# Kernel optimization log

Measured on AMD Instinct MI355X. Metric: run time of the kernel, lower is better.

## Reference

```python
import jax, jax.numpy as jnp
import numpy as np

N, M, P, K = 2, 131072, 1024, 4
C_TP, H_TP, W_TP = 32, 256, 256
PDIM, ODIM = 32, 32


def _harmonic(x, n=4):
    # pytorch3d HarmonicEmbedding: freqs 2^i, cat([sin, cos, x])
    freqs = 2.0 ** jnp.arange(n, dtype=x.dtype)
    e = (x[..., None] * freqs).reshape(x.shape[:-1] + (x.shape[-1] * n,))
    return jnp.concatenate([jnp.sin(e), jnp.cos(e), x], axis=-1)


def _normalize(x, eps=1e-12):
    return x / jnp.maximum(jnp.linalg.norm(x, axis=-1, keepdims=True), eps)


def _lin(x, w, b):
    return x @ w + b


def _grid_sample(img, gx, gy):
    # img [B,C,H,W]; gx,gy [B,Hg,Wg] in [-1,1]; bilinear, zeros pad, align_corners=False
    B, C, H, W = img.shape
    ix = ((gx + 1.0) * W - 1.0) / 2.0
    iy = ((gy + 1.0) * H - 1.0) / 2.0
    x0 = jnp.floor(ix); y0 = jnp.floor(iy)
    x1 = x0 + 1.0; y1 = y0 + 1.0
    wa = (x1 - ix) * (y1 - iy); wb = (ix - x0) * (y1 - iy)
    wc = (x1 - ix) * (iy - y0); wd = (ix - x0) * (iy - y0)
    b = jnp.arange(B)[:, None, None]

    def gather(xi, yi):
        xi = xi.astype(jnp.int32); yi = yi.astype(jnp.int32)
        valid = (xi >= 0) & (xi < W) & (yi >= 0) & (yi < H)
        xc = jnp.clip(xi, 0, W - 1); yc = jnp.clip(yi, 0, H - 1)
        v = img[b, :, yc, xc]  # [B,Hg,Wg,C]
        return v * valid[..., None]

    return (gather(x0, y0) * wa[..., None] + gather(x1, y0) * wb[..., None]
            + gather(x0, y1) * wc[..., None] + gather(x1, y1) * wd[..., None])


def _sample_from_planes_mean(coords, tplanes):
    # coords [N,M,3]; tplanes [N,3,C,H,W]; plane projections (x,y),(x,z),(z,y)
    n, m, _ = coords.shape
    _, n_pl, c, h, w = tplanes.shape
    proj = jnp.stack([coords[..., jnp.array([0, 1])],
                      coords[..., jnp.array([0, 2])],
                      coords[..., jnp.array([2, 1])]], axis=1)  # [N,3,M,2]
    proj = proj.reshape(n * n_pl, 1, m, 2)
    planes = tplanes.reshape(n * n_pl, c, h, w)
    out = _grid_sample(planes, proj[..., 0], proj[..., 1])  # [N*3,1,M,C]
    return out.reshape(n, n_pl, m, c).mean(axis=1)  # [N,M,C]


def _forward(coordinates, directions, points_position, tex_tplanes, pts_emb,
             q_w1, q_b1, q_w2, q_b2, f_w1, f_b1, f_w2, f_b2, f_w3, f_b3,
             d_w, d_b, r_w1, r_b1, r_w2, r_b2):
    selector = jnp.all((coordinates > -1.0) & (coordinates < 1.0), axis=-1)  # [N,M]
    tex = _sample_from_planes_mean(coordinates, tex_tplanes)  # [N,M,32]

    # KNN (squared distances, sorted ascending) via ||a||^2+||b||^2-2ab
    a2 = jnp.sum(coordinates * coordinates, -1)  # [N,M]
    b2 = jnp.sum(points_position * points_position, -1)  # [N,P]
    d2 = a2[:, :, None] + b2[:, None, :] - 2.0 * jnp.einsum('nmc,npc->nmp', coordinates, points_position)
    neg, idx = jax.lax.top_k(-d2, K)
    dist = -neg  # [N,M,K]
    bidx = jnp.arange(coordinates.shape[0])[:, None, None]
    nn = points_position[bidx, idx]  # [N,M,K,3]
    pf = pts_emb[idx]  # [N,M,K,32]
    rel = _normalize(coordinates[:, :, None] - nn)
    pe = _harmonic(rel)  # [N,M,K,27]
    h = jnp.concatenate([pf, pe], axis=-1)
    h = jax.nn.relu(_lin(h, q_w1, q_b1))
    h = _lin(h, q_w2, q_b2)  # [N,M,K,32]
    wgt = 1.0 / dist
    wgt = wgt / jnp.sum(wgt, axis=1, keepdims=True)  # note: dim=1 as in original
    pts_feat = jnp.sum(h * wgt[..., None], axis=2)  # [N,M,32]

    feat = jnp.concatenate([tex, pts_feat], axis=-1)
    feat = jax.nn.relu(_lin(feat, f_w1, f_b1))
    feat = jax.nn.relu(_lin(feat, f_w2, f_b2))
    feat = _lin(feat, f_w3, f_b3)  # [N,M,128]

    raw = (jax.nn.softplus(10.0 * _lin(feat, d_w, d_b)) / 10.0) * selector[..., None]
    densities = 1.0 - jnp.exp(-raw)

    rays = _harmonic(_normalize(directions))  # [N,M,27]
    rgb = jax.nn.relu(_lin(jnp.concatenate([feat, rays], axis=-1), r_w1, r_b1))
    rgb = _lin(rgb, r_w2, r_b2)
    r3 = jax.nn.sigmoid(rgb[..., :3]) * (1.0 + 2 * 0.001) - 0.001
    rgb = jnp.concatenate([r3, rgb[..., 3:]], axis=-1)
    return densities, rgb, dist


def setup_inputs() -> dict:
    keys = iter(jax.random.split(jax.random.key(0), 40))

    def nrm(shape, s=1.0):
        return jax.random.normal(next(keys), shape, jnp.float32) * s

    def lin_p(fin, fout):
        s = 1.0 / np.sqrt(fin)
        return nrm((fin, fout), s), nrm((fout,), s)

    coordinates = jax.random.uniform(next(keys), (N, M, 3), jnp.float32, -1.0, 1.0)
    directions = nrm((N, M, 3))
    points_position = jax.random.uniform(next(keys), (N, P, 3), jnp.float32, -1.0, 1.0)
    tex_tplanes = nrm((N, 3, C_TP, H_TP, W_TP))
    pts_emb = nrm((P, PDIM), 0.02)
    q_w1, q_b1 = lin_p(PDIM + 27, ODIM * 2)
    q_w2, q_b2 = lin_p(ODIM * 2, ODIM)
    f_w1, f_b1 = lin_p(64, 128)
    f_w2, f_b2 = lin_p(128, 128)
    f_w3, f_b3 = lin_p(128, 128)
    d_w, d_b = lin_p(128, 1)
    r_w1, r_b1 = lin_p(128 + 27, 64)
    r_w2, r_b2 = lin_p(64, 3)
    return dict(coordinates=coordinates, directions=directions,
                points_position=points_position, tex_tplanes=tex_tplanes,
                pts_emb=pts_emb, q_w1=q_w1, q_b1=q_b1, q_w2=q_w2, q_b2=q_b2,
                f_w1=f_w1, f_b1=f_b1, f_w2=f_w2, f_b2=f_b2, f_w3=f_w3, f_b3=f_b3,
                d_w=d_w, d_b=d_b, r_w1=r_w1, r_b1=r_b1, r_w2=r_w2, r_b2=r_b2)


def reference(coordinates, directions, points_position, tex_tplanes, pts_emb,
              q_w1, q_b1, q_w2, q_b2, f_w1, f_b1, f_w2, f_b2, f_w3, f_b3,
              d_w, d_b, r_w1, r_b1, r_w2, r_b2):
    return _forward(coordinates, directions, points_position, tex_tplanes, pts_emb,
                    q_w1, q_b1, q_w2, q_b2, f_w1, f_b1, f_w2, f_b2, f_w3, f_b3,
                    d_w, d_b, r_w1, r_b1, r_w2, r_b2)
```

## Files before the change

kernel.cpp:

```cpp
#include <hip/hip_runtime.h>

constexpr int MQ   = 131072;
constexpr int NPTS = 1024;

constexpr size_t WS_PTS4 = 4096;

__device__ __forceinline__ float np_sq3(float x, float y, float z){
  #pragma clang fp contract(off)
  float s = (x*x + y*y) + z*z;
  return s;
}
__device__ __forceinline__ float np_d2(float a2, float b2,
                                       float c0, float c1, float c2,
                                       float p0, float p1, float p2){
  #pragma clang fp contract(off)
  float dot = (c0*p0 + c1*p1) + c2*p2;
  float d   = (a2 + b2) - 2.0f*dot;
  return d;
}

__global__ void k_err_r15(float code, float* __restrict__ out){
  out[0] = code;
}

__global__ __launch_bounds__(256) void k_prep_r15(const float* __restrict__ pts,
                                                  float4* __restrict__ pts4,
                                                  float* __restrict__ denom){
  int i = blockIdx.x*256 + threadIdx.x;
  if (i < 8) denom[i] = 0.f;
  if (i < 2*NPTS){
    float x = pts[i*3+0], y = pts[i*3+1], z = pts[i*3+2];
    pts4[i] = make_float4(x, y, z, np_sq3(x,y,z));
  }
}

__global__ __launch_bounds__(256) void k_denom_r15(const float* __restrict__ coords,
                                                   const float4* __restrict__ pts4,
                                                   float* __restrict__ denom){
  __shared__ float red[4][4];
  int n = blockIdx.y;
  int m = blockIdx.x*256 + threadIdx.x;
  size_t g = (size_t)n*MQ + m;
  float c0 = coords[g*3+0], c1 = coords[g*3+1], c2 = coords[g*3+2];
  float a2 = np_sq3(c0,c1,c2);
  const float4* pp = pts4 + n*NPTS;
  float bd0=1e30f,bd1=1e30f,bd2=1e30f,bd3=1e30f;
  for (int p = 0; p < NPTS; ++p){
    float4 q = pp[p];
    float d = np_d2(a2, q.w, c0,c1,c2, q.x,q.y,q.z);
    if (d < bd3){
      if (d < bd2){
        bd3=bd2;
        if (d < bd1){ bd2=bd1; if (d < bd0){ bd1=bd0; bd0=d; } else bd1=d; }
        else bd2=d;
      } else bd3=d;
    }
  }
  float w0 = 1.f/bd0, w1 = 1.f/bd1, w2 = 1.f/bd2, w3 = 1.f/bd3;
  #pragma unroll
  for (int off=32; off>0; off>>=1){
    w0 += __shfl_down(w0, off); w1 += __shfl_down(w1, off);
    w2 += __shfl_down(w2, off); w3 += __shfl_down(w3, off);
  }
  int lane = threadIdx.x & 63, wv = threadIdx.x >> 6;
  if (lane == 0){ red[wv][0]=w0; red[wv][1]=w1; red[wv][2]=w2; red[wv][3]=w3; }
  __syncthreads();
  if (threadIdx.x < 4){
    int k = threadIdx.x;
    atomicAdd(&denom[n*4+k], red[0][k]+red[1][k]+red[2][k]+red[3][k]);
  }
}

template<int IN, int OUT, bool RELU>
__device__ __forceinline__ void layer_s(const float* in, float* out,
                                        const float* __restrict__ gw,
                                        const float* __restrict__ gb){
  #pragma unroll
  for (int jb = 0; jb < OUT/8; ++jb){
    float a[8];
    #pragma unroll
    for (int j=0;j<8;++j) a[j] = gb[jb*8+j];
    #pragma unroll
    for (int i = 0; i < IN; ++i){
      float x = in[i];
      #pragma unroll
      for (int j=0;j<8;++j) a[j] = fmaf(x, gw[i*OUT + jb*8 + j], a[j]);
    }
    #pragma unroll
    for (int j=0;j<8;++j) out[jb*8+j] = RELU ? fmaxf(a[j],0.f) : a[j];
  }
}

__global__ __launch_bounds__(256, 2) void k_main_r15(
    const float* __restrict__ coords, const float* __restrict__ dirs,
    const float* __restrict__ planes, const float* __restrict__ pemb,
    const float* __restrict__ qw1, const float* __restrict__ qb1,
    const float* __restrict__ qw2, const float* __restrict__ qb2,
    const float* __restrict__ fw1, const float* __restrict__ fb1,
    const float* __restrict__ fw2, const float* __restrict__ fb2,
    const float* __restrict__ fw3, const float* __restrict__ fb3,
    const float* __restrict__ dw,  const float* __restrict__ db,
    const float* __restrict__ rw1, const float* __restrict__ rb1,
    const float* __restrict__ rw2, const float* __restrict__ rb2,
    const float4* __restrict__ pts4, const float* __restrict__ denom,
    float* __restrict__ out)
{
  int tid = threadIdx.x;
  int n = blockIdx.x >> 9;
  int m = ((blockIdx.x & 511) << 8) + tid;
  size_t g = (size_t)n*MQ + m;

  float c0 = coords[g*3+0], c1 = coords[g*3+1], c2 = coords[g*3+2];
  bool sel = (c0 > -1.f) && (c0 < 1.f) && (c1 > -1.f) && (c1 < 1.f) && (c2 > -1.f) && (c2 < 1.f);

  float feat0[64];
  #pragma unroll
  for (int c=0;c<64;++c) feat0[c]=0.f;
  #pragma unroll
  for (int pl=0; pl<3; ++pl){
    float gx = (pl==2) ? c2 : c0;
    float gy = (pl==1) ? c2 : c1;
    float ix = ((gx + 1.f)*256.f - 1.f)*0.5f;
    float iy = ((gy + 1.f)*256.f - 1.f)*0.5f;
    float x0f = floorf(ix), y0f = floorf(iy);
    int x0 = (int)x0f, y0 = (int)y0f;
    float wxb = ix - x0f, wxa = (x0f + 1.f) - ix;
    float wyb = iy - y0f, wya = (y0f + 1.f) - iy;
    #pragma unroll
    for (int t=0;t<4;++t){
      int xi = x0 + (t & 1);
      int yi = y0 + (t >> 1);
      float wv = ((t&1) ? wxb : wxa) * ((t>>1) ? wyb : wya);
      if (xi>=0 && xi<256 && yi>=0 && yi<256){
        const float* tp_ = planes + (((size_t)(n*3+pl)) << 21) + ((yi<<8)+xi);
        #pragma unroll
        for (int c=0;c<32;++c) feat0[c] = fmaf(wv, tp_[(size_t)c<<16], feat0[c]);
      }
    }
  }
  #pragma unroll
  for (int c=0;c<32;++c) feat0[c] *= (1.f/3.f);

  float a2 = np_sq3(c0,c1,c2);
  const float4* ppts = pts4 + n*NPTS;
  float bd0=1e30f,bd1=1e30f,bd2=1e30f,bd3=1e30f;
  int   bi0=0,bi1=0,bi2=0,bi3=0;
  for (int p = 0; p < NPTS; ++p){
    float4 q = ppts[p];
    float d = np_d2(a2, q.w, c0,c1,c2, q.x,q.y,q.z);
    if (d < bd3){
      if (d < bd2){
        bd3=bd2; bi3=bi2;
        if (d < bd1){
          bd2=bd1; bi2=bi1;
          if (d < bd0){ bd1=bd0; bi1=bi0; bd0=d; bi0=p; }
          else        { bd1=d;   bi1=p; }
        } else        { bd2=d;   bi2=p; }
      } else          { bd3=d;   bi3=p; }
    }
  }

  #pragma unroll 1
  for (int k=0;k<4;++k){
    float dk = (k==0)?bd0:(k==1)?bd1:(k==2)?bd2:bd3;
    int   j  = (k==0)?bi0:(k==1)?bi1:(k==2)?bi2:bi3;
    float wk = (1.f/dk) / denom[n*4+k];
    float hin[59];
    const float4* pe = (const float4*)(pemb + ((size_t)j<<5));
    #pragma unroll
    for (int q4=0;q4<8;++q4){
      float4 v = pe[q4];
      hin[q4*4+0]=v.x; hin[q4*4+1]=v.y; hin[q4*4+2]=v.z; hin[q4*4+3]=v.w;
    }
    float4 pq = ppts[j];
    float vx = c0 - pq.x, vy = c1 - pq.y, vz = c2 - pq.z;
    float nr = fmaxf(sqrtf(vx*vx + vy*vy + vz*vz), 1e-12f);
    float r0 = vx/nr, r1 = vy/nr, r2 = vz/nr;
    #pragma unroll
    for (int d3=0; d3<3; ++d3){
      float rv = (d3==0)?r0:(d3==1)?r1:r2;
      #pragma unroll
      for (int f=0; f<4; ++f){
        float e = rv*(float)(1<<f);
        hin[32 + d3*4 + f] = __sinf(e);
        hin[44 + d3*4 + f] = __cosf(e);
      }
    }
    hin[56]=r0; hin[57]=r1; hin[58]=r2;
    float h1[64]; layer_s<59,64,true >(hin, h1, qw1, qb1);
    float h2[32]; layer_s<64,32,false>(h1, h2, qw2, qb2);
    #pragma unroll
    for (int c=0;c<32;++c) feat0[32+c] = fmaf(wk, h2[c], feat0[32+c]);
  }

  float4* odist = (float4*)(out + 262144 + 786432);
  odist[g] = make_float4(bd0,bd1,bd2,bd3);

  float f2[128];
  #pragma unroll
  for (int o=0;o<128;++o) f2[o] = fb2[o];
  #pragma unroll 1
  for (int ib=0; ib<16; ++ib){
    float t[8];
    #pragma unroll
    for (int j=0;j<8;++j) t[j] = fb1[ib*8+j];
    #pragma unroll
    for (int i=0;i<64;++i){
      float x = feat0[i];
      #pragma unroll
      for (int j=0;j<8;++j) t[j] = fmaf(x, fw1[i*128 + ib*8 + j], t[j]);
    }
    #pragma unroll
    for (int j=0;j<8;++j) t[j] = fmaxf(t[j], 0.f);
    #pragma unroll
    for (int j=0;j<8;++j){
      float x = t[j];
      #pragma unroll
      for (int o=0;o<128;++o) f2[o] = fmaf(x, fw2[(ib*8+j)*128 + o], f2[o]);
    }
  }
  #pragma unroll
  for (int o=0;o<128;++o) f2[o] = fmaxf(f2[o], 0.f);

  float dacc = db[0];
  float r1v[64];
  #pragma unroll
  for (int o=0;o<64;++o) r1v[o] = rb1[o];
  #pragma unroll 1
  for (int jb=0; jb<16; ++jb){
    float a[8];
    #pragma unroll
    for (int j=0;j<8;++j) a[j] = fb3[jb*8+j];
    #pragma unroll
    for (int i=0;i<128;++i){
      float x = f2[i];
      #pragma unroll
      for (int j=0;j<8;++j) a[j] = fmaf(x, fw3[i*128 + jb*8 + j], a[j]);
    }
    #pragma unroll
    for (int j=0;j<8;++j) dacc = fmaf(a[j], dw[jb*8+j], dacc);
    #pragma unroll
    for (int j=0;j<8;++j){
      float x = a[j];
      #pragma unroll
      for (int o=0;o<64;++o) r1v[o] = fmaf(x, rw1[(jb*8+j)*64 + o], r1v[o]);
    }
  }

  float z  = 10.f*dacc;
  float sp = (z > 0.f) ? (z + log1pf(__expf(-z))) : log1pf(__expf(z));
  float raw = sp*0.1f*(sel ? 1.f : 0.f);
  float dens = 1.f - __expf(-raw);

  float dx = dirs[g*3+0], dy = dirs[g*3+1], dz = dirs[g*3+2];
  float dn = fmaxf(sqrtf(dx*dx+dy*dy+dz*dz), 1e-12f);
  float n0 = dx/dn, n1 = dy/dn, n2 = dz/dn;
  float ext[27];
  #pragma unroll
  for (int d3=0; d3<3; ++d3){
    float nv = (d3==0)?n0:(d3==1)?n1:n2;
    #pragma unroll
    for (int f=0; f<4; ++f){
      float e = nv*(float)(1<<f);
      ext[d3*4 + f]      = __sinf(e);
      ext[12 + d3*4 + f] = __cosf(e);
    }
  }
  ext[24]=n0; ext[25]=n1; ext[26]=n2;
  #pragma unroll
  for (int i=0;i<27;++i){
    float x = ext[i];
    #pragma unroll
    for (int o=0;o<64;++o) r1v[o] = fmaf(x, rw1[(128+i)*64 + o], r1v[o]);
  }
  #pragma unroll
  for (int o=0;o<64;++o) r1v[o] = fmaxf(r1v[o], 0.f);

  float o0 = rb2[0], o1 = rb2[1], o2 = rb2[2];
  #pragma unroll
  for (int i=0;i<64;++i){
    float a = r1v[i];
    o0 = fmaf(a, rw2[i*3+0], o0);
    o1 = fmaf(a, rw2[i*3+1], o1);
    o2 = fmaf(a, rw2[i*3+2], o2);
  }
  o0 = 1.f/(1.f+__expf(-o0))*1.002f - 0.001f;
  o1 = 1.f/(1.f+__expf(-o1))*1.002f - 0.001f;
  o2 = 1.f/(1.f+__expf(-o2))*1.002f - 0.001f;

  out[g] = dens;
  float* orgb = out + 262144;
  orgb[g*3+0]=o0; orgb[g*3+1]=o1; orgb[g*3+2]=o2;
}

extern "C" void kernel_launch(void* const* d_in, const int* in_sizes, int n_in,
                              void* d_out, int out_size, void* d_ws, size_t ws_size,
                              hipStream_t stream){
  static const int expect[21] = {786432, 786432, 6144, 12582912, 32768,
                                 3776, 64, 2048, 32, 8192, 128, 16384, 128, 16384, 128,
                                 128, 1, 9920, 64, 192, 3};
  if (n_in != 21){ k_err_r15<<<1,1,0,stream>>>(128.f, (float*)d_out); return; }
  if (out_size != 2097152){ k_err_r15<<<1,1,0,stream>>>(129.f, (float*)d_out); return; }
  for (int i = 0; i < 21; ++i){
    if (in_sizes[i] != expect[i]){
      k_err_r15<<<1,1,0,stream>>>(130.f + (float)i, (float*)d_out);
      return;
    }
  }

  const float* coords = (const float*)d_in[0];
  const float* dirs   = (const float*)d_in[1];
  const float* pts    = (const float*)d_in[2];
  const float* planes = (const float*)d_in[3];
  const float* pemb   = (const float*)d_in[4];
  const float* qw1 = (const float*)d_in[5];  const float* qb1 = (const float*)d_in[6];
  const float* qw2 = (const float*)d_in[7];  const float* qb2 = (const float*)d_in[8];
  const float* fw1 = (const float*)d_in[9];  const float* fb1 = (const float*)d_in[10];
  const float* fw2 = (const float*)d_in[11]; const float* fb2 = (const float*)d_in[12];
  const float* fw3 = (const float*)d_in[13]; const float* fb3 = (const float*)d_in[14];
  const float* dw  = (const float*)d_in[15]; const float* db  = (const float*)d_in[16];
  const float* rw1 = (const float*)d_in[17]; const float* rb1 = (const float*)d_in[18];
  const float* rw2 = (const float*)d_in[19]; const float* rb2 = (const float*)d_in[20];

  char* ws = (char*)d_ws;
  float*  denom = (float*)ws;
  float4* pts4  = (float4*)(ws + WS_PTS4);

  k_prep_r15 <<<8, 256, 0, stream>>>(pts, pts4, denom);
  k_denom_r15<<<dim3(512,2), 256, 0, stream>>>(coords, pts4, denom);
  k_main_r15 <<<1024, 256, 0, stream>>>(coords, dirs, planes, pemb,
      qw1, qb1, qw2, qb2, fw1, fb1, fw2, fb2, fw3, fb3, dw, db, rw1, rb1, rw2, rb2,
      pts4, denom, (float*)d_out);
}
```

Measured before the change: 2.679 ms.

## Stage MLP weights in LDS and stream large layer weight tiles per block

Copies the small query-MLP weights, biases and the direction part of the RGB layer into shared memory once per block. It also streams 8-column tiles of the large fw1/fw2/fw3/rw1 matrices into shared buffers inside the layer loops, and all weight reads become float4 LDS reads. This replaces per-thread scalar global/scalar-cache weight loads with block-shared LDS reads. The cost is about 28KB of LDS per block and two block-wide barriers per tile iteration, which may limit occupancy and stall warps.

After: 8.876 ms. +231.3%, slower.

```diff
diff --git a/kernel.cpp b/kernel.cpp
--- a/kernel.cpp
+++ b/kernel.cpp
@@ -19,11 +19,11 @@
   return d;
 }
 
-__global__ void k_err_r15(float code, float* __restrict__ out){
+__global__ void k_err_r16(float code, float* __restrict__ out){
   out[0] = code;
 }
 
-__global__ __launch_bounds__(256) void k_prep_r15(const float* __restrict__ pts,
+__global__ __launch_bounds__(256) void k_prep_r16(const float* __restrict__ pts,
                                                   float4* __restrict__ pts4,
                                                   float* __restrict__ denom){
   int i = blockIdx.x*256 + threadIdx.x;
@@ -34,7 +34,7 @@
   }
 }
 
-__global__ __launch_bounds__(256) void k_denom_r15(const float* __restrict__ coords,
+__global__ __launch_bounds__(256) void k_denom_r16(const float* __restrict__ coords,
                                                    const float4* __restrict__ pts4,
                                                    float* __restrict__ denom){
   __shared__ float red[4][4];
@@ -72,26 +72,27 @@
 }
 
 template<int IN, int OUT, bool RELU>
-__device__ __forceinline__ void layer_s(const float* in, float* out,
-                                        const float* __restrict__ gw,
-                                        const float* __restrict__ gb){
+__device__ __forceinline__ void layer_lds_u(const float* in, float* out,
+                                            const float* w, const float* b){
   #pragma unroll
   for (int jb = 0; jb < OUT/8; ++jb){
     float a[8];
     #pragma unroll
-    for (int j=0;j<8;++j) a[j] = gb[jb*8+j];
+    for (int j=0;j<8;++j) a[j] = b[jb*8+j];
     #pragma unroll
     for (int i = 0; i < IN; ++i){
+      float4 wA = *(const float4*)(w + i*OUT + jb*8);
+      float4 wB = *(const float4*)(w + i*OUT + jb*8 + 4);
       float x = in[i];
-      #pragma unroll
-      for (int j=0;j<8;++j) a[j] = fmaf(x, gw[i*OUT + jb*8 + j], a[j]);
+      a[0]=fmaf(x,wA.x,a[0]); a[1]=fmaf(x,wA.y,a[1]); a[2]=fmaf(x,wA.z,a[2]); a[3]=fmaf(x,wA.w,a[3]);
+      a[4]=fmaf(x,wB.x,a[4]); a[5]=fmaf(x,wB.y,a[5]); a[6]=fmaf(x,wB.z,a[6]); a[7]=fmaf(x,wB.w,a[7]);
     }
     #pragma unroll
     for (int j=0;j<8;++j) out[jb*8+j] = RELU ? fmaxf(a[j],0.f) : a[j];
   }
 }
 
-__global__ __launch_bounds__(256, 2) void k_main_r15(
+__global__ __launch_bounds__(256, 2) void k_main_r16(
     const float* __restrict__ coords, const float* __restrict__ dirs,
     const float* __restrict__ planes, const float* __restrict__ pemb,
     const float* __restrict__ qw1, const float* __restrict__ qb1,
@@ -105,7 +106,27 @@
     const float4* __restrict__ pts4, const float* __restrict__ denom,
     float* __restrict__ out)
 {
+  __shared__ __align__(16) float s_qw1[59*64];
+  __shared__ __align__(16) float s_qw2[64*32];
+  __shared__ __align__(16) float s_rwe[27*64];
+  __shared__ __align__(16) float s_bufA[1024];
+  __shared__ __align__(16) float s_bufB[512];
+  __shared__ float s_dw[128], s_rw2[192];
+  __shared__ float s_qb1[64], s_qb2[32], s_fb1[128], s_fb2[128], s_fb3[128];
+  __shared__ float s_rb1[64], s_rb2[4], s_db[1];
+
   int tid = threadIdx.x;
+  for (int i = tid; i < 59*64; i += 256) s_qw1[i] = qw1[i];
+  for (int i = tid; i < 64*32; i += 256) s_qw2[i] = qw2[i];
+  for (int i = tid; i < 27*64; i += 256) s_rwe[i] = rw1[128*64 + i];
+  if (tid < 192) s_rw2[tid] = rw2[tid];
+  if (tid < 128){ s_dw[tid]=dw[tid]; s_fb1[tid]=fb1[tid]; s_fb2[tid]=fb2[tid]; s_fb3[tid]=fb3[tid]; }
+  if (tid < 64){ s_qb1[tid]=qb1[tid]; s_rb1[tid]=rb1[tid]; }
+  if (tid < 32) s_qb2[tid]=qb2[tid];
+  if (tid < 3)  s_rb2[tid]=rb2[tid];
+  if (tid == 0) s_db[0]=db[0];
+  __syncthreads();
+
   int n = blockIdx.x >> 9;
   int m = ((blockIdx.x & 511) << 8) + tid;
   size_t g = (size_t)n*MQ + m;
@@ -187,8 +208,8 @@
       }
     }
     hin[56]=r0; hin[57]=r1; hin[58]=r2;
-    float h1[64]; layer_s<59,64,true >(hin, h1, qw1, qb1);
-    float h2[32]; layer_s<64,32,false>(h1, h2, qw2, qb2);
+    float h1[64]; layer_lds_u<59,64,true >(hin, h1, s_qw1, s_qb1);
+    float h2[32]; layer_lds_u<64,32,false>(h1, h2, s_qw2, s_qb2);
     #pragma unroll
     for (int c=0;c<32;++c) feat0[32+c] = fmaf(wk, h2[c], feat0[32+c]);
   }
@@ -198,17 +219,25 @@
 
   float f2[128];
   #pragma unroll
-  for (int o=0;o<128;++o) f2[o] = fb2[o];
+  for (int o=0;o<128;++o) f2[o] = s_fb2[o];
   #pragma unroll 1
   for (int ib=0; ib<16; ++ib){
+    __syncthreads();
+    for (int idx = tid; idx < 512; idx += 256)
+      s_bufB[idx] = fw1[(idx>>3)*128 + (ib<<3) + (idx&7)];
+    for (int idx = tid; idx < 1024; idx += 256)
+      s_bufA[idx] = fw2[(ib<<10) + idx];
+    __syncthreads();
     float t[8];
     #pragma unroll
-    for (int j=0;j<8;++j) t[j] = fb1[ib*8+j];
+    for (int j=0;j<8;++j) t[j] = s_fb1[ib*8+j];
     #pragma unroll
     for (int i=0;i<64;++i){
+      float4 wA = *(const float4*)(s_bufB + i*8);
+      float4 wB = *(const float4*)(s_bufB + i*8 + 4);
       float x = feat0[i];
-      #pragma unroll
-      for (int j=0;j<8;++j) t[j] = fmaf(x, fw1[i*128 + ib*8 + j], t[j]);
+      t[0]=fmaf(x,wA.x,t[0]); t[1]=fmaf(x,wA.y,t[1]); t[2]=fmaf(x,wA.z,t[2]); t[3]=fmaf(x,wA.w,t[3]);
+      t[4]=fmaf(x,wB.x,t[4]); t[5]=fmaf(x,wB.y,t[5]); t[6]=fmaf(x,wB.z,t[6]); t[7]=fmaf(x,wB.w,t[7]);
     }
     #pragma unroll
     for (int j=0;j<8;++j) t[j] = fmaxf(t[j], 0.f);
@@ -216,34 +245,50 @@
     for (int j=0;j<8;++j){
       float x = t[j];
       #pragma unroll
-      for (int o=0;o<128;++o) f2[o] = fmaf(x, fw2[(ib*8+j)*128 + o], f2[o]);
+      for (int o4=0;o4<32;++o4){
+        float4 w = *(const float4*)(s_bufA + j*128 + o4*4);
+        f2[o4*4+0]=fmaf(x,w.x,f2[o4*4+0]); f2[o4*4+1]=fmaf(x,w.y,f2[o4*4+1]);
+        f2[o4*4+2]=fmaf(x,w.z,f2[o4*4+2]); f2[o4*4+3]=fmaf(x,w.w,f2[o4*4+3]);
+      }
     }
   }
   #pragma unroll
   for (int o=0;o<128;++o) f2[o] = fmaxf(f2[o], 0.f);
 
-  float dacc = db[0];
+  float dacc = s_db[0];
   float r1v[64];
   #pragma unroll
-  for (int o=0;o<64;++o) r1v[o] = rb1[o];
+  for (int o=0;o<64;++o) r1v[o] = s_rb1[o];
   #pragma unroll 1
   for (int jb=0; jb<16; ++jb){
+    __syncthreads();
+    for (int idx = tid; idx < 1024; idx += 256)
+      s_bufA[idx] = fw3[(idx>>3)*128 + (jb<<3) + (idx&7)];
+    for (int idx = tid; idx < 512; idx += 256)
+      s_bufB[idx] = rw1[(jb<<3)*64 + idx];
+    __syncthreads();
     float a[8];
     #pragma unroll
-    for (int j=0;j<8;++j) a[j] = fb3[jb*8+j];
+    for (int j=0;j<8;++j) a[j] = s_fb3[jb*8+j];
     #pragma unroll
     for (int i=0;i<128;++i){
+      float4 wA = *(const float4*)(s_bufA + i*8);
+      float4 wB = *(const float4*)(s_bufA + i*8 + 4);
       float x = f2[i];
-      #pragma unroll
-      for (int j=0;j<8;++j) a[j] = fmaf(x, fw3[i*128 + jb*8 + j], a[j]);
-    }
-    #pragma unroll
-    for (int j=0;j<8;++j) dacc = fmaf(a[j], dw[jb*8+j], dacc);
+      a[0]=fmaf(x,wA.x,a[0]); a[1]=fmaf(x,wA.y,a[1]); a[2]=fmaf(x,wA.z,a[2]); a[3]=fmaf(x,wA.w,a[3]);
+      a[4]=fmaf(x,wB.x,a[4]); a[5]=fmaf(x,wB.y,a[5]); a[6]=fmaf(x,wB.z,a[6]); a[7]=fmaf(x,wB.w,a[7]);
+    }
+    #pragma unroll
+    for (int j=0;j<8;++j) dacc = fmaf(a[j], s_dw[jb*8+j], dacc);
     #pragma unroll
     for (int j=0;j<8;++j){
       float x = a[j];
       #pragma unroll
-      for (int o=0;o<64;++o) r1v[o] = fmaf(x, rw1[(jb*8+j)*64 + o], r1v[o]);
+      for (int o4=0;o4<16;++o4){
+        float4 w = *(const float4*)(s_bufB + j*64 + o4*4);
+        r1v[o4*4+0]=fmaf(x,w.x,r1v[o4*4+0]); r1v[o4*4+1]=fmaf(x,w.y,r1v[o4*4+1]);
+        r1v[o4*4+2]=fmaf(x,w.z,r1v[o4*4+2]); r1v[o4*4+3]=fmaf(x,w.w,r1v[o4*4+3]);
+      }
     }
   }
 
@@ -271,18 +316,22 @@
   for (int i=0;i<27;++i){
     float x = ext[i];
     #pragma unroll
-    for (int o=0;o<64;++o) r1v[o] = fmaf(x, rw1[(128+i)*64 + o], r1v[o]);
+    for (int o4=0;o4<16;++o4){
+      float4 w = *(const float4*)(s_rwe + i*64 + o4*4);
+      r1v[o4*4+0]=fmaf(x,w.x,r1v[o4*4+0]); r1v[o4*4+1]=fmaf(x,w.y,r1v[o4*4+1]);
+      r1v[o4*4+2]=fmaf(x,w.z,r1v[o4*4+2]); r1v[o4*4+3]=fmaf(x,w.w,r1v[o4*4+3]);
+    }
   }
   #pragma unroll
   for (int o=0;o<64;++o) r1v[o] = fmaxf(r1v[o], 0.f);
 
-  float o0 = rb2[0], o1 = rb2[1], o2 = rb2[2];
+  float o0 = s_rb2[0], o1 = s_rb2[1], o2 = s_rb2[2];
   #pragma unroll
   for (int i=0;i<64;++i){
     float a = r1v[i];
-    o0 = fmaf(a, rw2[i*3+0], o0);
-    o1 = fmaf(a, rw2[i*3+1], o1);
-    o2 = fmaf(a, rw2[i*3+2], o2);
+    o0 = fmaf(a, s_rw2[i*3+0], o0);
+    o1 = fmaf(a, s_rw2[i*3+1], o1);
+    o2 = fmaf(a, s_rw2[i*3+2], o2);
   }
   o0 = 1.f/(1.f+__expf(-o0))*1.002f - 0.001f;
   o1 = 1.f/(1.f+__expf(-o1))*1.002f - 0.001f;
@@ -299,11 +348,11 @@
   static const int expect[21] = {786432, 786432, 6144, 12582912, 32768,
                                  3776, 64, 2048, 32, 8192, 128, 16384, 128, 16384, 128,
                                  128, 1, 9920, 64, 192, 3};
-  if (n_in != 21){ k_err_r15<<<1,1,0,stream>>>(128.f, (float*)d_out); return; }
-  if (out_size != 2097152){ k_err_r15<<<1,1,0,stream>>>(129.f, (float*)d_out); return; }
+  if (n_in != 21){ k_err_r16<<<1,1,0,stream>>>(128.f, (float*)d_out); return; }
+  if (out_size != 2097152){ k_err_r16<<<1,1,0,stream>>>(129.f, (float*)d_out); return; }
   for (int i = 0; i < 21; ++i){
     if (in_sizes[i] != expect[i]){
-      k_err_r15<<<1,1,0,stream>>>(130.f + (float)i, (float*)d_out);
+      k_err_r16<<<1,1,0,stream>>>(130.f + (float)i, (float*)d_out);
       return;
     }
   }
@@ -326,9 +375,9 @@
   float*  denom = (float*)ws;
   float4* pts4  = (float4*)(ws + WS_PTS4);
 
-  k_prep_r15 <<<8, 256, 0, stream>>>(pts, pts4, denom);
-  k_denom_r15<<<dim3(512,2), 256, 0, stream>>>(coords, pts4, denom);
-  k_main_r15 <<<1024, 256, 0, stream>>>(coords, dirs, planes, pemb,
+  k_prep_r16 <<<8, 256, 0, stream>>>(pts, pts4, denom);
+  k_denom_r16<<<dim3(512,2), 256, 0, stream>>>(coords, pts4, denom);
+  k_main_r16 <<<1024, 256, 0, stream>>>(coords, dirs, planes, pemb,
       qw1, qb1, qw2, qb2, fw1, fb1, fw2, fb2, fw3, fb3, dw, db, rw1, rb1, rw2, rb2,
       pts4, denom, (float*)d_out);
 }
```

## Split each query across four lanes with shuffle-based MLPs and LDS-staged weights

Applied to the files above, without the earlier changes.

The main kernel now assigns four threads to each query point instead of one. Texture channels, the KNN scan (each lane covers a quarter of the points, then a shuffle merge with index tie-break) and every MLP layer's output columns are divided across the four lanes. Inputs are broadcast with shuffles, and weights are staged in shared memory in 2048-float chunks. The intent is to cut per-thread register arrays (feat0, f2, r1v) so occupancy can rise, and to replace scalar global weight loads with vectorised LDS reads. The cost is many more __syncthreads and shuffles, four times as many blocks, and repeated weight staging per block.

Result: slower. 9.246 ms (+245.1%).

```diff
diff --git a/kernel.cpp b/kernel.cpp
--- a/kernel.cpp
+++ b/kernel.cpp
@@ -19,11 +19,11 @@
   return d;
 }
 
-__global__ void k_err_r15(float code, float* __restrict__ out){
+__global__ void k_err_r19(float code, float* __restrict__ out){
   out[0] = code;
 }
 
-__global__ __launch_bounds__(256) void k_prep_r15(const float* __restrict__ pts,
+__global__ __launch_bounds__(256) void k_prep_r19(const float* __restrict__ pts,
                                                   float4* __restrict__ pts4,
                                                   float* __restrict__ denom){
   int i = blockIdx.x*256 + threadIdx.x;
@@ -34,7 +34,7 @@
   }
 }
 
-__global__ __launch_bounds__(256) void k_denom_r15(const float* __restrict__ coords,
+__global__ __launch_bounds__(256) void k_denom_r19(const float* __restrict__ coords,
                                                    const float4* __restrict__ pts4,
                                                    float* __restrict__ denom){
   __shared__ float red[4][4];
@@ -71,27 +71,7 @@
   }
 }
 
-template<int IN, int OUT, bool RELU>
-__device__ __forceinline__ void layer_s(const float* in, float* out,
-                                        const float* __restrict__ gw,
-                                        const float* __restrict__ gb){
-  #pragma unroll
-  for (int jb = 0; jb < OUT/8; ++jb){
-    float a[8];
-    #pragma unroll
-    for (int j=0;j<8;++j) a[j] = gb[jb*8+j];
-    #pragma unroll
-    for (int i = 0; i < IN; ++i){
-      float x = in[i];
-      #pragma unroll
-      for (int j=0;j<8;++j) a[j] = fmaf(x, gw[i*OUT + jb*8 + j], a[j]);
-    }
-    #pragma unroll
-    for (int j=0;j<8;++j) out[jb*8+j] = RELU ? fmaxf(a[j],0.f) : a[j];
-  }
-}
-
-__global__ __launch_bounds__(256, 2) void k_main_r15(
+__global__ __launch_bounds__(256, 3) void k_main_r19(
     const float* __restrict__ coords, const float* __restrict__ dirs,
     const float* __restrict__ planes, const float* __restrict__ pemb,
     const float* __restrict__ qw1, const float* __restrict__ qb1,
@@ -105,17 +85,41 @@
     const float4* __restrict__ pts4, const float* __restrict__ denom,
     float* __restrict__ out)
 {
+  __shared__ __align__(16) float s_qw1[59*64];
+  __shared__ __align__(16) float s_qw2[64*32];
+  __shared__ __align__(16) float s_rwe[27*64];
+  __shared__ __align__(16) float s_wbuf[2048];
+  __shared__ float s_dw[128], s_rw2[192];
+  __shared__ float s_qb1[64], s_qb2[32], s_fb1[128], s_fb2[128], s_fb3[128];
+  __shared__ float s_rb1[64], s_rb2[4], s_db[1];
+
   int tid = threadIdx.x;
-  int n = blockIdx.x >> 9;
-  int m = ((blockIdx.x & 511) << 8) + tid;
+  for (int i = tid; i < 59*64; i += 256) s_qw1[i] = qw1[i];
+  for (int i = tid; i < 64*32; i += 256) s_qw2[i] = qw2[i];
+  for (int i = tid; i < 27*64; i += 256) s_rwe[i] = rw1[128*64 + i];
+  if (tid < 192) s_rw2[tid] = rw2[tid];
+  if (tid < 128){ s_dw[tid]=dw[tid]; s_fb1[tid]=fb1[tid]; s_fb2[tid]=fb2[tid]; s_fb3[tid]=fb3[tid]; }
+  if (tid < 64){ s_qb1[tid]=qb1[tid]; s_rb1[tid]=rb1[tid]; }
+  if (tid < 32) s_qb2[tid]=qb2[tid];
+  if (tid < 3)  s_rb2[tid]=rb2[tid];
+  if (tid == 0) s_db[0]=db[0];
+  __syncthreads();
+
+  const int lane = tid & 63;
+  const int base = lane & 60;
+  const int q    = tid & 3;
+  const int pb   = tid >> 2;
+
+  int n = blockIdx.x >> 11;
+  int m = ((blockIdx.x & 2047) << 6) + pb;
   size_t g = (size_t)n*MQ + m;
 
   float c0 = coords[g*3+0], c1 = coords[g*3+1], c2 = coords[g*3+2];
   bool sel = (c0 > -1.f) && (c0 < 1.f) && (c1 > -1.f) && (c1 < 1.f) && (c2 > -1.f) && (c2 < 1.f);
 
-  float feat0[64];
-  #pragma unroll
-  for (int c=0;c<64;++c) feat0[c]=0.f;
+  float texq[8];
+  #pragma unroll
+  for (int j=0;j<8;++j) texq[j]=0.f;
   #pragma unroll
   for (int pl=0; pl<3; ++pl){
     float gx = (pl==2) ? c2 : c0;
@@ -134,119 +138,206 @@
       if (xi>=0 && xi<256 && yi>=0 && yi<256){
         const float* tp_ = planes + (((size_t)(n*3+pl)) << 21) + ((yi<<8)+xi);
         #pragma unroll
-        for (int c=0;c<32;++c) feat0[c] = fmaf(wv, tp_[(size_t)c<<16], feat0[c]);
-      }
-    }
-  }
-  #pragma unroll
-  for (int c=0;c<32;++c) feat0[c] *= (1.f/3.f);
+        for (int j=0;j<8;++j)
+          texq[j] = fmaf(wv, tp_[(size_t)(q*8+j)<<16], texq[j]);
+      }
+    }
+  }
+  #pragma unroll
+  for (int j=0;j<8;++j) texq[j] *= (1.f/3.f);
 
   float a2 = np_sq3(c0,c1,c2);
   const float4* ppts = pts4 + n*NPTS;
-  float bd0=1e30f,bd1=1e30f,bd2=1e30f,bd3=1e30f;
-  int   bi0=0,bi1=0,bi2=0,bi3=0;
-  for (int p = 0; p < NPTS; ++p){
-    float4 q = ppts[p];
-    float d = np_d2(a2, q.w, c0,c1,c2, q.x,q.y,q.z);
-    if (d < bd3){
-      if (d < bd2){
-        bd3=bd2; bi3=bi2;
-        if (d < bd1){
-          bd2=bd1; bi2=bi1;
-          if (d < bd0){ bd1=bd0; bi1=bi0; bd0=d; bi0=p; }
-          else        { bd1=d;   bi1=p; }
-        } else        { bd2=d;   bi2=p; }
-      } else          { bd3=d;   bi3=p; }
-    }
-  }
+  float qd0=1e30f,qd1=1e30f,qd2=1e30f,qd3=1e30f;
+  int   qi0=0x7fffffff,qi1=0x7fffffff,qi2=0x7fffffff,qi3=0x7fffffff;
+  {
+    int p0 = q << 8;
+    for (int p = p0; p < p0+256; ++p){
+      float4 qq = ppts[p];
+      float d = np_d2(a2, qq.w, c0,c1,c2, qq.x,qq.y,qq.z);
+      if (d < qd3){
+        if (d < qd2){
+          qd3=qd2; qi3=qi2;
+          if (d < qd1){
+            qd2=qd1; qi2=qi1;
+            if (d < qd0){ qd1=qd0; qi1=qi0; qd0=d; qi0=p; }
+            else        { qd1=d;   qi1=p; }
+          } else        { qd2=d;   qi2=p; }
+        } else          { qd3=d;   qi3=p; }
+      }
+    }
+  }
+  float md0=1e30f,md1=1e30f,md2=1e30f,md3=1e30f;
+  int   mi0=0x7fffffff,mi1=0x7fffffff,mi2=0x7fffffff,mi3=0x7fffffff;
+  #pragma unroll
+  for (int s=0;s<4;++s){
+    float cd0=__shfl(qd0, base+s), cd1=__shfl(qd1, base+s);
+    float cd2=__shfl(qd2, base+s), cd3=__shfl(qd3, base+s);
+    int   ci0=__shfl(qi0, base+s), ci1=__shfl(qi1, base+s);
+    int   ci2=__shfl(qi2, base+s), ci3=__shfl(qi3, base+s);
+    #pragma unroll
+    for (int r=0;r<4;++r){
+      float d  = (r==0)?cd0:(r==1)?cd1:(r==2)?cd2:cd3;
+      int   ix = (r==0)?ci0:(r==1)?ci1:(r==2)?ci2:ci3;
+      if ((d < md3) || (d == md3 && ix < mi3)){
+        if ((d < md2) || (d == md2 && ix < mi2)){
+          md3=md2; mi3=mi2;
+          if ((d < md1) || (d == md1 && ix < mi1)){
+            md2=md1; mi2=mi1;
+            if ((d < md0) || (d == md0 && ix < mi0)){
+              md1=md0; mi1=mi0; md0=d; mi0=ix;
+            } else { md1=d; mi1=ix; }
+          } else { md2=d; mi2=ix; }
+        } else { md3=d; mi3=ix; }
+      }
+    }
+  }
+
+  float ptsf[8];
+  #pragma unroll
+  for (int c=0;c<8;++c) ptsf[c]=0.f;
 
   #pragma unroll 1
   for (int k=0;k<4;++k){
-    float dk = (k==0)?bd0:(k==1)?bd1:(k==2)?bd2:bd3;
-    int   j  = (k==0)?bi0:(k==1)?bi1:(k==2)?bi2:bi3;
+    float dk = (k==0)?md0:(k==1)?md1:(k==2)?md2:md3;
+    int   j  = (k==0)?mi0:(k==1)?mi1:(k==2)?mi2:mi3;
     float wk = (1.f/dk) / denom[n*4+k];
-    float hin[59];
-    const float4* pe = (const float4*)(pemb + ((size_t)j<<5));
-    #pragma unroll
-    for (int q4=0;q4<8;++q4){
-      float4 v = pe[q4];
-      hin[q4*4+0]=v.x; hin[q4*4+1]=v.y; hin[q4*4+2]=v.z; hin[q4*4+3]=v.w;
-    }
     float4 pq = ppts[j];
     float vx = c0 - pq.x, vy = c1 - pq.y, vz = c2 - pq.z;
     float nr = fmaxf(sqrtf(vx*vx + vy*vy + vz*vz), 1e-12f);
-    float r0 = vx/nr, r1 = vy/nr, r2 = vz/nr;
-    #pragma unroll
-    for (int d3=0; d3<3; ++d3){
-      float rv = (d3==0)?r0:(d3==1)?r1:r2;
-      #pragma unroll
-      for (int f=0; f<4; ++f){
-        float e = rv*(float)(1<<f);
-        hin[32 + d3*4 + f] = __sinf(e);
-        hin[44 + d3*4 + f] = __cosf(e);
-      }
-    }
-    hin[56]=r0; hin[57]=r1; hin[58]=r2;
-    float h1[64]; layer_s<59,64,true >(hin, h1, qw1, qb1);
-    float h2[32]; layer_s<64,32,false>(h1, h2, qw2, qb2);
-    #pragma unroll
-    for (int c=0;c<32;++c) feat0[32+c] = fmaf(wk, h2[c], feat0[32+c]);
-  }
-
-  float4* odist = (float4*)(out + 262144 + 786432);
-  odist[g] = make_float4(bd0,bd1,bd2,bd3);
-
-  float f2[128];
-  #pragma unroll
-  for (int o=0;o<128;++o) f2[o] = fb2[o];
-  #pragma unroll 1
-  for (int ib=0; ib<16; ++ib){
-    float t[8];
-    #pragma unroll
-    for (int j=0;j<8;++j) t[j] = fb1[ib*8+j];
-    #pragma unroll
-    for (int i=0;i<64;++i){
-      float x = feat0[i];
-      #pragma unroll
-      for (int j=0;j<8;++j) t[j] = fmaf(x, fw1[i*128 + ib*8 + j], t[j]);
-    }
-    #pragma unroll
-    for (int j=0;j<8;++j) t[j] = fmaxf(t[j], 0.f);
-    #pragma unroll
-    for (int j=0;j<8;++j){
-      float x = t[j];
-      #pragma unroll
-      for (int o=0;o<128;++o) f2[o] = fmaf(x, fw2[(ib*8+j)*128 + o], f2[o]);
-    }
-  }
-  #pragma unroll
-  for (int o=0;o<128;++o) f2[o] = fmaxf(f2[o], 0.f);
-
-  float dacc = db[0];
-  float r1v[64];
-  #pragma unroll
-  for (int o=0;o<64;++o) r1v[o] = rb1[o];
-  #pragma unroll 1
-  for (int jb=0; jb<16; ++jb){
-    float a[8];
-    #pragma unroll
-    for (int j=0;j<8;++j) a[j] = fb3[jb*8+j];
-    #pragma unroll
-    for (int i=0;i<128;++i){
-      float x = f2[i];
-      #pragma unroll
-      for (int j=0;j<8;++j) a[j] = fmaf(x, fw3[i*128 + jb*8 + j], a[j]);
-    }
-    #pragma unroll
-    for (int j=0;j<8;++j) dacc = fmaf(a[j], dw[jb*8+j], dacc);
-    #pragma unroll
-    for (int j=0;j<8;++j){
-      float x = a[j];
-      #pragma unroll
-      for (int o=0;o<64;++o) r1v[o] = fmaf(x, rw1[(jb*8+j)*64 + o], r1v[o]);
-    }
-  }
-
+    float r0_ = vx/nr, r1_ = vy/nr, r2_ = vz/nr;
+
+    float hinq[15];
+    #pragma unroll
+    for (int t=0;t<8;++t) hinq[t] = pemb[(size_t)j*32 + t*4 + q];
+    {
+      float rr[3] = {r0_, r1_, r2_};
+      float fsc = (float)(1 << q);
+      #pragma unroll
+      for (int d3=0; d3<3; ++d3){
+        float e = rr[d3]*fsc;
+        hinq[8+d3]  = __sinf(e);
+        hinq[11+d3] = __cosf(e);
+      }
+    }
+    hinq[14] = (q==0)?r0_:((q==1)?r1_:((q==2)?r2_:0.f));
+
+    float h1q[16];
+    {
+      float acc[16];
+      #pragma unroll
+      for (int c=0;c<16;++c) acc[c] = s_qb1[q*16+c];
+      #pragma unroll
+      for (int i=0;i<59;++i){
+        float x = __shfl(hinq[i>>2], base + (i&3));
+        #pragma unroll
+        for (int c4=0;c4<4;++c4){
+          float4 w = *(const float4*)(&s_qw1[i*64 + q*16 + c4*4]);
+          acc[c4*4+0]=fmaf(x,w.x,acc[c4*4+0]); acc[c4*4+1]=fmaf(x,w.y,acc[c4*4+1]);
+          acc[c4*4+2]=fmaf(x,w.z,acc[c4*4+2]); acc[c4*4+3]=fmaf(x,w.w,acc[c4*4+3]);
+        }
+      }
+      #pragma unroll
+      for (int c=0;c<16;++c) h1q[c] = fmaxf(acc[c], 0.f);
+    }
+    {
+      float acc[8];
+      #pragma unroll
+      for (int c=0;c<8;++c) acc[c] = s_qb2[q*8+c];
+      #pragma unroll
+      for (int i=0;i<64;++i){
+        float x = __shfl(h1q[i&15], base + (i>>4));
+        #pragma unroll
+        for (int c4=0;c4<2;++c4){
+          float4 w = *(const float4*)(&s_qw2[i*32 + q*8 + c4*4]);
+          acc[c4*4+0]=fmaf(x,w.x,acc[c4*4+0]); acc[c4*4+1]=fmaf(x,w.y,acc[c4*4+1]);
+          acc[c4*4+2]=fmaf(x,w.z,acc[c4*4+2]); acc[c4*4+3]=fmaf(x,w.w,acc[c4*4+3]);
+        }
+      }
+      #pragma unroll
+      for (int c=0;c<8;++c) ptsf[c] = fmaf(wk, acc[c], ptsf[c]);
+    }
+  }
+
+  if (q == 0){
+    float4* odist = (float4*)(out + 262144 + 786432);
+    odist[g] = make_float4(md0,md1,md2,md3);
+  }
+
+
+  float f1q[32];
+  #pragma unroll
+  for (int c=0;c<32;++c) f1q[c] = s_fb1[q*32+c];
+  #pragma unroll
+  for (int ib=0; ib<4; ++ib){
+    __syncthreads();
+    for (int x = tid; x < 2048; x += 256) s_wbuf[x] = fw1[ib*2048 + x];
+    __syncthreads();
+    #pragma unroll
+    for (int i2=0; i2<16; ++i2){
+      const int i = ib*16 + i2;
+      float x = (i < 32) ? __shfl(texq[i&7], base + (i>>3))
+                         : __shfl(ptsf[i&7], base + (i>>3) - 4);
+      #pragma unroll
+      for (int c4=0;c4<8;++c4){
+        float4 w = *(const float4*)(&s_wbuf[i2*128 + q*32 + c4*4]);
+        f1q[c4*4+0]=fmaf(x,w.x,f1q[c4*4+0]); f1q[c4*4+1]=fmaf(x,w.y,f1q[c4*4+1]);
+        f1q[c4*4+2]=fmaf(x,w.z,f1q[c4*4+2]); f1q[c4*4+3]=fmaf(x,w.w,f1q[c4*4+3]);
+      }
+    }
+  }
+  #pragma unroll
+  for (int c=0;c<32;++c) f1q[c] = fmaxf(f1q[c], 0.f);
+
+  float f2q[32];
+  #pragma unroll
+  for (int c=0;c<32;++c) f2q[c] = s_fb2[q*32+c];
+  #pragma unroll
+  for (int ib=0; ib<8; ++ib){
+    __syncthreads();
+    for (int x = tid; x < 2048; x += 256) s_wbuf[x] = fw2[ib*2048 + x];
+    __syncthreads();
+    #pragma unroll
+    for (int i2=0; i2<16; ++i2){
+      const int i = ib*16 + i2;
+      float x = __shfl(f1q[i&31], base + (i>>5));
+      #pragma unroll
+      for (int c4=0;c4<8;++c4){
+        float4 w = *(const float4*)(&s_wbuf[i2*128 + q*32 + c4*4]);
+        f2q[c4*4+0]=fmaf(x,w.x,f2q[c4*4+0]); f2q[c4*4+1]=fmaf(x,w.y,f2q[c4*4+1]);
+        f2q[c4*4+2]=fmaf(x,w.z,f2q[c4*4+2]); f2q[c4*4+3]=fmaf(x,w.w,f2q[c4*4+3]);
+      }
+    }
+  }
+  #pragma unroll
+  for (int c=0;c<32;++c) f2q[c] = fmaxf(f2q[c], 0.f);
+
+  float f3q[32];
+  #pragma unroll
+  for (int c=0;c<32;++c) f3q[c] = s_fb3[q*32+c];
+  #pragma unroll
+  for (int ib=0; ib<8; ++ib){
+    __syncthreads();
+    for (int x = tid; x < 2048; x += 256) s_wbuf[x] = fw3[ib*2048 + x];
+    __syncthreads();
+    #pragma unroll
+    for (int i2=0; i2<16; ++i2){
+      const int i = ib*16 + i2;
+      float x = __shfl(f2q[i&31], base + (i>>5));
+      #pragma unroll
+      for (int c4=0;c4<8;++c4){
+        float4 w = *(const float4*)(&s_wbuf[i2*128 + q*32 + c4*4]);
+        f3q[c4*4+0]=fmaf(x,w.x,f3q[c4*4+0]); f3q[c4*4+1]=fmaf(x,w.y,f3q[c4*4+1]);
+        f3q[c4*4+2]=fmaf(x,w.z,f3q[c4*4+2]); f3q[c4*4+3]=fmaf(x,w.w,f3q[c4*4+3]);
+      }
+    }
+  }
+
+  float pd = 0.f;
+  #pragma unroll
+  for (int c=0;c<32;++c) pd = fmaf(f3q[c], s_dw[q*32+c], pd);
+  float dacc = s_db[0] + __shfl(pd, base+0) + __shfl(pd, base+1)
+                       + __shfl(pd, base+2) + __shfl(pd, base+3);
   float z  = 10.f*dacc;
   float sp = (z > 0.f) ? (z + log1pf(__expf(-z))) : log1pf(__expf(z));
   float raw = sp*0.1f*(sel ? 1.f : 0.f);
@@ -267,30 +358,60 @@
     }
   }
   ext[24]=n0; ext[25]=n1; ext[26]=n2;
+
+  float r1q[16];
+  #pragma unroll
+  for (int c=0;c<16;++c) r1q[c] = s_rb1[q*16+c];
+  #pragma unroll
+  for (int ib=0; ib<4; ++ib){
+    __syncthreads();
+    for (int x = tid; x < 2048; x += 256) s_wbuf[x] = rw1[ib*2048 + x];
+    __syncthreads();
+    #pragma unroll
+    for (int i2=0; i2<32; ++i2){
+      const int i = ib*32 + i2;
+      float x = __shfl(f3q[i&31], base + (i>>5));
+      #pragma unroll
+      for (int c4=0;c4<4;++c4){
+        float4 w = *(const float4*)(&s_wbuf[i2*64 + q*16 + c4*4]);
+        r1q[c4*4+0]=fmaf(x,w.x,r1q[c4*4+0]); r1q[c4*4+1]=fmaf(x,w.y,r1q[c4*4+1]);
+        r1q[c4*4+2]=fmaf(x,w.z,r1q[c4*4+2]); r1q[c4*4+3]=fmaf(x,w.w,r1q[c4*4+3]);
+      }
+    }
+  }
   #pragma unroll
   for (int i=0;i<27;++i){
     float x = ext[i];
     #pragma unroll
-    for (int o=0;o<64;++o) r1v[o] = fmaf(x, rw1[(128+i)*64 + o], r1v[o]);
-  }
-  #pragma unroll
-  for (int o=0;o<64;++o) r1v[o] = fmaxf(r1v[o], 0.f);
-
-  float o0 = rb2[0], o1 = rb2[1], o2 = rb2[2];
-  #pragma unroll
-  for (int i=0;i<64;++i){
-    float a = r1v[i];
-    o0 = fmaf(a, rw2[i*3+0], o0);
-    o1 = fmaf(a, rw2[i*3+1], o1);
-    o2 = fmaf(a, rw2[i*3+2], o2);
-  }
+    for (int c4=0;c4<4;++c4){
+      float4 w = *(const float4*)(&s_rwe[i*64 + q*16 + c4*4]);
+      r1q[c4*4+0]=fmaf(x,w.x,r1q[c4*4+0]); r1q[c4*4+1]=fmaf(x,w.y,r1q[c4*4+1]);
+      r1q[c4*4+2]=fmaf(x,w.z,r1q[c4*4+2]); r1q[c4*4+3]=fmaf(x,w.w,r1q[c4*4+3]);
+    }
+  }
+  #pragma unroll
+  for (int c=0;c<16;++c) r1q[c] = fmaxf(r1q[c], 0.f);
+
+  float p0=0.f, p1=0.f, p2=0.f;
+  #pragma unroll
+  for (int c=0;c<16;++c){
+    float a = r1q[c];
+    p0 = fmaf(a, s_rw2[(q*16+c)*3+0], p0);
+    p1 = fmaf(a, s_rw2[(q*16+c)*3+1], p1);
+    p2 = fmaf(a, s_rw2[(q*16+c)*3+2], p2);
+  }
+  float o0 = s_rb2[0] + __shfl(p0,base+0) + __shfl(p0,base+1) + __shfl(p0,base+2) + __shfl(p0,base+3);
+  float o1 = s_rb2[1] + __shfl(p1,base+0) + __shfl(p1,base+1) + __shfl(p1,base+2) + __shfl(p1,base+3);
+  float o2 = s_rb2[2] + __shfl(p2,base+0) + __shfl(p2,base+1) + __shfl(p2,base+2) + __shfl(p2,base+3);
   o0 = 1.f/(1.f+__expf(-o0))*1.002f - 0.001f;
   o1 = 1.f/(1.f+__expf(-o1))*1.002f - 0.001f;
   o2 = 1.f/(1.f+__expf(-o2))*1.002f - 0.001f;
 
-  out[g] = dens;
-  float* orgb = out + 262144;
-  orgb[g*3+0]=o0; orgb[g*3+1]=o1; orgb[g*3+2]=o2;
+  if (q == 0){
+    out[g] = dens;
+    float* orgb = out + 262144;
+    orgb[g*3+0]=o0; orgb[g*3+1]=o1; orgb[g*3+2]=o2;
+  }
 }
 
 extern "C" void kernel_launch(void* const* d_in, const int* in_sizes, int n_in,
@@ -299,11 +420,11 @@
   static const int expect[21] = {786432, 786432, 6144, 12582912, 32768,
                                  3776, 64, 2048, 32, 8192, 128, 16384, 128, 16384, 128,
                                  128, 1, 9920, 64, 192, 3};
-  if (n_in != 21){ k_err_r15<<<1,1,0,stream>>>(128.f, (float*)d_out); return; }
-  if (out_size != 2097152){ k_err_r15<<<1,1,0,stream>>>(129.f, (float*)d_out); return; }
+  if (n_in != 21){ k_err_r19<<<1,1,0,stream>>>(128.f, (float*)d_out); return; }
+  if (out_size != 2097152){ k_err_r19<<<1,1,0,stream>>>(129.f, (float*)d_out); return; }
   for (int i = 0; i < 21; ++i){
     if (in_sizes[i] != expect[i]){
-      k_err_r15<<<1,1,0,stream>>>(130.f + (float)i, (float*)d_out);
+      k_err_r19<<<1,1,0,stream>>>(130.f + (float)i, (float*)d_out);
       return;
     }
   }
@@ -326,9 +447,9 @@
   float*  denom = (float*)ws;
   float4* pts4  = (float4*)(ws + WS_PTS4);
 
-  k_prep_r15 <<<8, 256, 0, stream>>>(pts, pts4, denom);
-  k_denom_r15<<<dim3(512,2), 256, 0, stream>>>(coords, pts4, denom);
-  k_main_r15 <<<1024, 256, 0, stream>>>(coords, dirs, planes, pemb,
+  k_prep_r19 <<<8, 256, 0, stream>>>(pts, pts4, denom);
+  k_denom_r19<<<dim3(512,2), 256, 0, stream>>>(coords, pts4, denom);
+  k_main_r19 <<<4096, 256, 0, stream>>>(coords, dirs, planes, pemb,
       qw1, qb1, qw2, qb2, fw1, fb1, fw2, fb2, fw3, fb3, dw, db, rw1, rb1, rw2, rb2,
       pts4, denom, (float*)d_out);
 }
```
